# Performance work log

Measured on AMD Instinct MI355X. Metric: run time of the kernel, lower is better.

## Reference

```python
import jax, jax.numpy as jnp
import numpy as np

K = 8                      # batch_k
NONZERO_CUTOFF = 1.4       # nonzero_loss_cutoff
MARGIN = 1.0               # F.triplet_margin_loss default (module's margin arg is unused)
PD_EPS = 1e-6              # torch pairwise_distance eps


def setup_inputs() -> dict:
    key = jax.random.key(0)
    x = jax.random.normal(key, (4096, 128), dtype=jnp.float32)
    return {"x": x}


def _sample_indices(x, key):
    """Distance-weighted negative sampling; returns (a_idx, p_idx, n_idx), each [n*(K-1)]."""
    n, d = x.shape
    # per-row L2 normalize (eps added to norm, as in original)
    xn = x / (jnp.sqrt(jnp.sum(x * x, axis=1, keepdims=True)) + 1e-5)
    # pairwise euclidean distance; identity added under sqrt exactly as original
    sq = jnp.sum(xn * xn, axis=1, keepdims=True)               # [n,1]
    dist2 = sq + sq.T - 2.0 * (xn @ xn.T)                       # [n,n]
    dist = jnp.sqrt(dist2 + jnp.eye(n, dtype=x.dtype))          # [n,n]
    # distance-weighted sampling log-weights (Wu et al.)
    log_w = (2.0 - d) * jnp.log(dist) - (d - 3) / 2.0 * jnp.log(1.0 - 0.25 * dist * dist)
    w = jnp.exp(log_w - jnp.max(log_w))
    # block mask: same-block pairs excluded
    block = jnp.arange(n) // K                                  # [n]
    mask = (block[:, None] != block[None, :]).astype(x.dtype)
    w = w * mask * (dist < NONZERO_CUTOFF).astype(x.dtype)
    row_sum = jnp.sum(w, axis=1, keepdims=True)
    # rows where weights are degenerate fall back to uniform (original's try/except)
    valid = jnp.isfinite(row_sum) & (row_sum > 0) & jnp.all(jnp.isfinite(w), axis=1, keepdims=True)
    logits = jnp.where(valid, jnp.where(w > 0, jnp.log(w), -jnp.inf), 0.0)   # [n,n]
    # batched categorical sampling via Gumbel-max: K-1 negatives per anchor
    g = jax.random.gumbel(key, (n, K - 1, n), dtype=jnp.float32)
    n_idx = jnp.argmax(logits[:, None, :] + g, axis=-1).reshape(-1)          # [n*(K-1)]
    # anchor/positive pairs: for each i, all other members of its block
    r = jnp.arange(n) % K                                       # position in block
    off = jnp.arange(K - 1)
    p_off = jnp.where(off[None, :] < r[:, None], off[None, :], off[None, :] + 1)
    p_idx = (block[:, None] * K + p_off).reshape(-1)            # [n*(K-1)]
    a_idx = jnp.repeat(jnp.arange(n), K - 1)                    # [n*(K-1)]
    return a_idx, p_idx, n_idx


def reference(x) -> jnp.ndarray:
    key = jax.random.key(42)
    a_idx, p_idx, n_idx = _sample_indices(x, key)
    a, p, ng = x[a_idx], x[p_idx], x[n_idx]
    d_ap = jnp.sqrt(jnp.sum((a - p + PD_EPS) ** 2, axis=1))
    d_an = jnp.sqrt(jnp.sum((a - ng + PD_EPS) ** 2, axis=1))
    return jnp.mean(jnp.maximum(d_ap - d_an + MARGIN, 0.0))
```

## Files before the change

kernel.cpp:

```cpp
#include <hip/hip_runtime.h>
#include <stdint.h>

#define NROWS 4096
#define DIM   128
#define KB    8
#define NS    7
#define TCH   16
#define NPAIR 2048
#define HALF_CNT 58720256u

typedef __bf16 v8bf __attribute__((ext_vector_type(8)));
typedef float  v4f  __attribute__((ext_vector_type(4)));

__device__ __forceinline__ uint32_t rotl32(uint32_t x, int r) {
    return __builtin_amdgcn_alignbit(x, x, 32 - r);
}

__device__ __forceinline__ void threefry2x32(uint32_t c0, uint32_t c1,
                                             uint32_t& o0, uint32_t& o1) {
    const uint32_t ks0 = 0u;
    const uint32_t ks1 = 42u;
    const uint32_t ks2 = 0x1BD11BDAu ^ ks0 ^ ks1;
    uint32_t x0 = c0 + ks0;
    uint32_t x1 = c1 + ks1;
#define TF_R(r) { x0 += x1; x1 = rotl32(x1, r); x1 ^= x0; }
    TF_R(13) TF_R(15) TF_R(26) TF_R(6)
    x0 += ks1; x1 += ks2 + 1u;
    TF_R(17) TF_R(29) TF_R(16) TF_R(24)
    x0 += ks2; x1 += ks0 + 2u;
    TF_R(13) TF_R(15) TF_R(26) TF_R(6)
    x0 += ks0; x1 += ks1 + 3u;
    TF_R(17) TF_R(29) TF_R(16) TF_R(24)
    x0 += ks1; x1 += ks2 + 4u;
    TF_R(13) TF_R(15) TF_R(26) TF_R(6)
    x0 += ks2; x1 += ks0 + 5u;
#undef TF_R
    o0 = x0; o1 = x1;
}

__device__ __forceinline__ float gumbel_of(uint32_t b) {
    float f = __uint_as_float((b >> 9) | 0x3f800000u) - 1.0f;
    float u = f + 1.17549435e-38f;
    float l1 = __log2f(u);
    float inner = -0.69314718055994531f * l1;
    float l2 = __log2f(inner);
    return -0.69314718055994531f * l2;
}

__global__ void knorm(const float* __restrict__ x, __bf16* __restrict__ xb,
                      float* __restrict__ sqv) {
    const int i = blockIdx.x;
    const int t = threadIdx.x;
    float2 v = ((const float2*)(x + (size_t)i * DIM))[t];
    float s = v.x * v.x + v.y * v.y;
#pragma unroll
    for (int m = 32; m > 0; m >>= 1) s += __shfl_xor(s, m, 64);
    float norm = sqrtf(s) + 1e-5f;
    float ox = v.x / norm, oy = v.y / norm;
    union { __bf16 b[2]; uint32_t u; } ph;
    ph.b[0] = (__bf16)ox; ph.b[1] = (__bf16)oy;
    ((uint32_t*)xb)[i * 64 + t] = ph.u;
    float s2 = ox * ox + oy * oy;
#pragma unroll
    for (int m = 32; m > 0; m >>= 1) s2 += __shfl_xor(s2, m, 64);
    if (t == 0) sqv[i] = s2;
}

__global__ __launch_bounds__(256, 4) void kdist(
        const __bf16* __restrict__ xb, const float* __restrict__ sqv,
        int* __restrict__ cnt, unsigned short* __restrict__ t16,
        float2* __restrict__ nwp) {
    const int lane  = threadIdx.x & 63;
    const int chunk = (blockIdx.x << 2) + (threadIdx.x >> 6);
    const int grp   = blockIdx.y;
    const int rlo = lane & 15;
    const int khi = lane >> 4;
    const unsigned int below = (1u << rlo) - 1u;

    const int afr = grp * 8 + (rlo >> 1) + ((rlo & 1) << 11);
    v8bf ah[4];
#pragma unroll
    for (int ks = 0; ks < 4; ++ks)
        ah[ks] = *(const v8bf*)(xb + (size_t)afr * DIM + ks * 32 + khi * 8);

    const int base = grp * 8 + khi * 2;
    float sqA[4];
    sqA[0] = sqv[base];
    sqA[1] = sqv[base + 2048];
    sqA[2] = sqv[base + 1];
    sqA[3] = sqv[base + 2049];

    const int rbA = ((base)     * 16 + chunk) << 8;
    const int rbB = ((base + 1) * 16 + chunk) << 8;
    unsigned int cA = 0, cB = 0;

    const int tcol0 = chunk * 256 + rlo;

    v8bf bhn[4];
    float sqn;
    {
        const size_t boff = (size_t)tcol0 * DIM + khi * 8;
#pragma unroll
        for (int ks = 0; ks < 4; ++ks) bhn[ks] = *(const v8bf*)(xb + boff + ks * 32);
        sqn = sqv[tcol0];
    }

#pragma unroll 1
    for (int cg = 0; cg < 16; ++cg) {
        v8bf bhc[4];
#pragma unroll
        for (int ks = 0; ks < 4; ++ks) bhc[ks] = bhn[ks];
        const float sqB = sqn;
        const int tcol = tcol0 + cg * 16;

        if (cg < 15) {
            const size_t boff = (size_t)(tcol + 16) * DIM + khi * 8;
#pragma unroll
            for (int ks = 0; ks < 4; ++ks) bhn[ks] = *(const v8bf*)(xb + boff + ks * 32);
            sqn = sqv[tcol + 16];
        }

        v4f acc = {0.f, 0.f, 0.f, 0.f};
#pragma unroll
        for (int ks = 0; ks < 4; ++ks)
            acc = __builtin_amdgcn_mfma_f32_16x16x32_bf16(ah[ks], bhc[ks], acc, 0, 0, 0);

        const int tBlk = tcol >> 3;
        const bool bd0 = (tBlk != grp);
        const bool bd1 = (tBlk != grp + 256);

        float nw[4];
        bool  ic[4];
#pragma unroll
        for (int q = 0; q < 4; ++q) {
            float d2  = fmaf(-2.0f, acc[q], sqA[q] + sqB);
            float l1  = __log2f(d2);
            float t2  = fmaf(-0.25f, d2, 1.0f);
            float l2  = __log2f(t2);
            float wiv = exp2f(fmaf(63.0f, l1, 62.5f * l2));
            bool incl = (d2 < 1.96f) && ((q & 1) ? bd1 : bd0);
            ic[q] = incl;
            nw[q] = incl ? -wiv : -INFINITY;
        }

        const bool uA = ic[0] | ic[1];
        const bool uB = ic[2] | ic[3];
        unsigned long long ballA = __ballot(uA);
        unsigned long long ballB = __ballot(uB);
        unsigned int subA = (unsigned int)((ballA >> (khi * 16)) & 0xFFFFull);
        unsigned int subB = (unsigned int)((ballB >> (khi * 16)) & 0xFFFFull);
        if (uA) {
            int slot = rbA + (int)cA + __popc(subA & below);
            t16[slot] = (unsigned short)tcol;
            nwp[slot] = make_float2(nw[0], nw[1]);
        }
        if (uB) {
            int slot = rbB + (int)cB + __popc(subB & below);
            t16[slot] = (unsigned short)tcol;
            nwp[slot] = make_float2(nw[2], nw[3]);
        }
        cA += (unsigned int)__popc(subA);
        cB += (unsigned int)__popc(subB);
    }

    if (rlo == 0) {
        cnt[base * 16 + chunk]       = (int)cA;
        cnt[(base + 1) * 16 + chunk] = (int)cB;
    }
}

__global__ __launch_bounds__(256, 8) void kgum(
        const int* __restrict__ cnt, const unsigned short* __restrict__ t16,
        const float2* __restrict__ nwp,
        unsigned long long* __restrict__ pk) {
    const int wid  = threadIdx.x >> 6;
    const int rid  = (blockIdx.x << 2) + wid;
    const int p    = rid >> 4;
    const int lane = threadIdx.x & 63;
    const int j    = lane & 7;
    const int eo   = lane >> 3;
    const bool jv  = (j < 7);
    const uint32_t pb = ((uint32_t)p * 7u + (uint32_t)j) << 12;

    __shared__ unsigned short st[4][256];
    __shared__ float2         snw[4][256];

    const int n  = cnt[rid];
    const int rb = rid << 8;

    for (int s = lane; s < n; s += 64) {
        st[wid][s]  = t16[rb + s];
        snw[wid][s] = nwp[rb + s];
    }
    __syncthreads();

    unsigned long long bA = ~0ull, bB = ~0ull;

#pragma unroll 1
    for (int e = eo; e < n; e += 8) {
        const uint32_t t = st[wid][e];
        const float2 nw  = snw[wid][e];
        const uint32_t L = pb + t;
        uint32_t o0, o1;
        threefry2x32(L, L + HALF_CNT, o0, o1);
        float fA = __uint_as_float((o0 >> 9) | 0x3f800000u) - 1.0f;
        float fB = __uint_as_float((o1 >> 9) | 0x3f800000u) - 1.0f;
        float l1A = __log2f(fA + 1.17549435e-38f);
        float l1B = __log2f(fB + 1.17549435e-38f);
        float kA = jv ? l1A * nw.x : INFINITY;
        float kB = jv ? l1B * nw.y : INFINITY;
        unsigned long long pA = ((unsigned long long)__float_as_uint(kA) << 32) | t;
        unsigned long long pB = ((unsigned long long)__float_as_uint(kB) << 32) | t;
        bA = pA < bA ? pA : bA;
        bB = pB < bB ? pB : bB;
    }

#pragma unroll
    for (int m = 8; m < 64; m <<= 1) {
        unsigned long long vA = __shfl_xor(bA, m, 64);
        unsigned long long vB = __shfl_xor(bB, m, 64);
        bA = vA < bA ? vA : bA;
        bB = vB < bB ? vB : bB;
    }

    if (eo == 0 && jv) {
        atomicMin(&pk[(size_t)p * NS + j], bA);
        atomicMin(&pk[(size_t)(p + 2048) * NS + j], bB);
    }
}

__global__ void kextract(const unsigned long long* __restrict__ pk,
                         int* __restrict__ nidx) {
    int s = blockIdx.x * 256 + threadIdx.x;
    if (s >= NROWS * NS) return;
    unsigned long long v = pk[s];
    uint32_t kb = (uint32_t)(v >> 32);
    nidx[s] = (kb >= 0x7F800000u) ? -1 : (int)(v & 0xFFFFu);
}

__global__ __launch_bounds__(256, 2) void ksample(
        const __bf16* __restrict__ xb, const float* __restrict__ sqv,
        float* __restrict__ pV, int* __restrict__ pI) {
    const int lane  = threadIdx.x & 63;
    const int chunk = (blockIdx.x << 2) + (threadIdx.x >> 6);
    const int grp   = blockIdx.y;
    const int rlo = lane & 15;
    const int khi = lane >> 4;

    const int afr = grp * 8 + (rlo >> 1) + ((rlo & 1) << 11);
    v8bf ah[4];
#pragma unroll
    for (int ks = 0; ks < 4; ++ks)
        ah[ks] = *(const v8bf*)(xb + (size_t)afr * DIM + ks * 32 + khi * 8);
    const int base = grp * 8 + khi * 2;
    float sqA[4];
    sqA[0] = sqv[base];
    sqA[1] = sqv[base + 2048];
    sqA[2] = sqv[base + 1];
    sqA[3] = sqv[base + 2049];
    const uint32_t P0 = (uint32_t)base;
    const uint32_t P1 = (uint32_t)(base + 1);

    float    bestV[4][NS];
    uint32_t bestP[4];
#pragma unroll
    for (int q = 0; q < 4; ++q) {
        bestP[q] = 0u;
#pragma unroll
        for (int j = 0; j < NS; ++j) bestV[q][j] = INFINITY;
    }
    const int tcol0 = chunk * 256 + rlo;

    v8bf bhn[4];
    float sqn;
    {
        const size_t boff = (size_t)tcol0 * DIM + khi * 8;
#pragma unroll
        for (int ks = 0; ks < 4; ++ks) bhn[ks] = *(const v8bf*)(xb + boff + ks * 32);
        sqn = sqv[tcol0];
    }

#pragma unroll 1
    for (int cg = 0; cg < 16; ++cg) {
        v8bf bhc[4];
#pragma unroll
        for (int ks = 0; ks < 4; ++ks) bhc[ks] = bhn[ks];
        const float sqB = sqn;
        const int tcol = tcol0 + cg * 16;
        if (cg < 15) {
            const size_t boff = (size_t)(tcol + 16) * DIM + khi * 8;
#pragma unroll
            for (int ks = 0; ks < 4; ++ks) bhn[ks] = *(const v8bf*)(xb + boff + ks * 32);
            sqn = sqv[tcol + 16];
        }
        v4f acc = {0.f, 0.f, 0.f, 0.f};
#pragma unroll
        for (int ks = 0; ks < 4; ++ks)
            acc = __builtin_amdgcn_mfma_f32_16x16x32_bf16(ah[ks], bhc[ks], acc, 0, 0, 0);
        const int tBlk = tcol >> 3;
        const bool bd0 = (tBlk != grp);
        const bool bd1 = (tBlk != grp + 256);
        float nw[4];
#pragma unroll
        for (int q = 0; q < 4; ++q) {
            float d2  = fmaf(-2.0f, acc[q], sqA[q] + sqB);
            float l1  = __log2f(d2);
            float t2  = fmaf(-0.25f, d2, 1.0f);
            float l2  = __log2f(t2);
            float wiv = exp2f(fmaf(63.0f, l1, 62.5f * l2));
            bool incl = (d2 < 1.96f) && ((q & 1) ? bd1 : bd0);
            nw[q] = incl ? -wiv : -INFINITY;
        }
        const uint32_t tB = (uint32_t)tcol;
#pragma unroll
        for (int j = 0; j < NS; ++j) {
            uint32_t L0 = ((P0 * 7u + (uint32_t)j) << 12) + tB;
            uint32_t L1 = ((P1 * 7u + (uint32_t)j) << 12) + tB;
            uint32_t o0, o1, o2, o3;
            threefry2x32(L0, L0 + HALF_CNT, o0, o1);
            threefry2x32(L1, L1 + HALF_CNT, o2, o3);
            float vv[4];
            vv[0] = __log2f(__uint_as_float((o0 >> 9) | 0x3f800000u) - 1.0f + 1.17549435e-38f) * nw[0];
            vv[1] = __log2f(__uint_as_float((o1 >> 9) | 0x3f800000u) - 1.0f + 1.17549435e-38f) * nw[1];
            vv[2] = __log2f(__uint_as_float((o2 >> 9) | 0x3f800000u) - 1.0f + 1.17549435e-38f) * nw[2];
            vv[3] = __log2f(__uint_as_float((o3 >> 9) | 0x3f800000u) - 1.0f + 1.17549435e-38f) * nw[3];
            const uint32_t keep = ~(0xFu << (4 * j));
            const uint32_t put  = ((uint32_t)cg) << (4 * j);
#pragma unroll
            for (int q = 0; q < 4; ++q) {
                bool lt = vv[q] < bestV[q][j];
                uint32_t np = (bestP[q] & keep) | put;
                bestV[q][j] = lt ? vv[q] : bestV[q][j];
                bestP[q]    = lt ? np : bestP[q];
            }
        }
    }
#pragma unroll
    for (int q = 0; q < 4; ++q) {
        const int a = base + (q >> 1) + ((q & 1) << 11);
#pragma unroll
        for (int j = 0; j < NS; ++j) {
            float v = bestV[q][j];
            int idx = tcol0 + (int)((bestP[q] >> (4 * j)) & 0xFu) * 16;
#pragma unroll
            for (int m = 1; m < 16; m <<= 1) {
                float v2 = __shfl_xor(v, m, 16);
                int   i2 = __shfl_xor(idx, m, 16);
                if (v2 < v || (v2 == v && i2 < idx)) { v = v2; idx = i2; }
            }
            if (rlo == 0) {
                size_t s = ((size_t)a * NS + j) * TCH + chunk;
                pV[s] = v;
                pI[s] = idx;
            }
        }
    }
}

__global__ void kcombine(const float* __restrict__ pV, const int* __restrict__ pI,
                         int* __restrict__ nidx, int nc) {
    int s = blockIdx.x * 256 + threadIdx.x;
    if (s >= NROWS * NS) return;
    float bv = INFINITY;
    int bi = 0x7FFFFFFF;
    for (int c = 0; c < nc; ++c) {
        float v = pV[(size_t)s * nc + c];
        int idx = pI[(size_t)s * nc + c];
        if (v < bv || (v == bv && idx < bi)) { bv = v; bi = idx; }
    }
    nidx[s] = (bv == INFINITY) ? -1 : bi;
}

__global__ void kfixup(int* __restrict__ nidx) {
    const int i = blockIdx.x;
    if (nidx[(size_t)i * NS] >= 0) return;
    const int lane = threadIdx.x;
    for (int j = 0; j < NS; ++j) {
        float bv = -INFINITY;
        int bi = 0x7FFFFFFF;
        for (int t = lane; t < NROWS; t += 64) {
            uint32_t o0, o1;
            float g;
            if (i < 2048) {
                uint32_t L = (((uint32_t)(i * NS + j)) << 12) + (uint32_t)t;
                threefry2x32(L, L + HALF_CNT, o0, o1);
                g = gumbel_of(o0);
            } else {
                uint32_t L = (((uint32_t)((i - 2048) * NS + j)) << 12) + (uint32_t)t;
                threefry2x32(L, L + HALF_CNT, o0, o1);
                g = gumbel_of(o1);
            }
            if (g > bv) { bv = g; bi = t; }
        }
#pragma unroll
        for (int m = 1; m < 64; m <<= 1) {
            float v2 = __shfl_xor(bv, m, 64);
            int   i2 = __shfl_xor(bi, m, 64);
            if (v2 > bv || (v2 == bv && i2 < bi)) { bv = v2; bi = i2; }
        }
        if (lane == 0) nidx[i * NS + j] = bi;
    }
}

__global__ void kloss(const float* __restrict__ x, const int* __restrict__ nidx,
                      float* __restrict__ loss) {
    int s = blockIdx.x * 256 + threadIdx.x;
    if (s >= NROWS * NS) return;
    int i = s / NS, j = s - i * NS;
    int r = i & (KB - 1), blk = i >> 3;
    int po = (j < r) ? j : j + 1;
    int p = blk * KB + po;
    int n = nidx[s] & (NROWS - 1);
    const float4* A  = (const float4*)(x + (size_t)i * DIM);
    const float4* P  = (const float4*)(x + (size_t)p * DIM);
    const float4* Ng = (const float4*)(x + (size_t)n * DIM);
    float sap = 0.0f, san = 0.0f;
#pragma unroll 8
    for (int k = 0; k < DIM / 4; ++k) {
        float4 a = A[k], pv = P[k], nv = Ng[k];
        float d;
        d = a.x - pv.x + 1e-6f; sap += d * d;
        d = a.y - pv.y + 1e-6f; sap += d * d;
        d = a.z - pv.z + 1e-6f; sap += d * d;
        d = a.w - pv.w + 1e-6f; sap += d * d;
        d = a.x - nv.x + 1e-6f; san += d * d;
        d = a.y - nv.y + 1e-6f; san += d * d;
        d = a.z - nv.z + 1e-6f; san += d * d;
        d = a.w - nv.w + 1e-6f; san += d * d;
    }
    loss[s] = fmaxf(sqrtf(sap) - sqrtf(san) + 1.0f, 0.0f);
}

__global__ void kreduce(const float* __restrict__ loss, float* __restrict__ out) {
    __shared__ float part[4];
    const int tid = threadIdx.x;
    float sum = 0.0f;
    for (int s = tid; s < NROWS * NS; s += 256) sum += loss[s];
#pragma unroll
    for (int m = 32; m > 0; m >>= 1) sum += __shfl_xor(sum, m, 64);
    if ((tid & 63) == 0) part[tid >> 6] = sum;
    __syncthreads();
    if (tid == 0) out[0] = (part[0] + part[1] + part[2] + part[3]) / 28672.0f;
}

extern "C" void kernel_launch(void* const* d_in, const int* in_sizes, int n_in,
                              void* d_out, int out_size, void* d_ws, size_t ws_size,
                              hipStream_t stream) {
    const float* x = (const float*)d_in[0];
    float* out = (float*)d_out;

    uint8_t* w = (uint8_t*)d_ws;
    size_t off = 0;
    auto take = [&](size_t bytes) {
        void* p = w + off;
        off = (off + bytes + 255) & ~(size_t)255;
        return p;
    };
    __bf16* xb   = (__bf16*)take((size_t)NROWS * DIM * 2);
    float*  sqv  = (float*)take((size_t)NROWS * 4);
    int*    nidx = (int*)take((size_t)NROWS * NS * 4);
    float*  loss = (float*)take((size_t)NROWS * NS * 4);
    int*    cnt  = (int*)take((size_t)NPAIR * 16 * 4);
    unsigned long long* pk = (unsigned long long*)take((size_t)NROWS * NS * 8);
    const size_t prefix = off;
    const size_t t16_b = (size_t)NPAIR * 16 * 256 * 2;
    const size_t nwp_b = (size_t)NPAIR * 16 * 256 * 8;
    const size_t NEED_BIG = prefix + ((t16_b + 255) & ~(size_t)255)
                          + ((nwp_b + 255) & ~(size_t)255);

    knorm<<<NROWS, 64, 0, stream>>>(x, xb, sqv);

    if (ws_size >= NEED_BIG) {
        unsigned short* t16 = (unsigned short*)take(t16_b);
        float2*         nwp = (float2*)take(nwp_b);
        hipMemsetAsync(pk, 0xFF, (size_t)NROWS * NS * 8, stream);
        kdist<<<dim3(TCH / 4, 256), 256, 0, stream>>>(xb, sqv, cnt, t16, nwp);
        kgum<<<NPAIR * 16 / 4, 256, 0, stream>>>(cnt, t16, nwp, pk);
        kextract<<<(NROWS * NS + 255) / 256, 256, 0, stream>>>(pk, nidx);
    } else {
        float* pV = (float*)take((size_t)NROWS * NS * TCH * 4);
        int*   pI = (int*)take((size_t)NROWS * NS * TCH * 4);
        ksample<<<dim3(TCH / 4, 256), 256, 0, stream>>>(xb, sqv, pV, pI);
        kcombine<<<(NROWS * NS + 255) / 256, 256, 0, stream>>>(pV, pI, nidx, TCH);
    }

    kfixup<<<NROWS, 64, 0, stream>>>(nidx);
    kloss<<<(NROWS * NS + 255) / 256, 256, 0, stream>>>(x, nidx, loss);
    kreduce<<<1, 256, 0, stream>>>(loss, out);
}
```

Baseline: 198.8 us.

## Restructure Gumbel kernel to one block per pair, drop atomics and extract pass

The Gumbel-max kernel now assigns one block per anchor pair. Each thread loops over all 7 samples for each candidate, so every candidate is loaded once instead of through a lane-per-sample split that left one of eight lanes idle. Per-sample minima are reduced with wave shuffles and then across waves in shared memory, and the block writes nidx directly. This removes the memset, the 64-bit global atomicMin and the separate extract kernel. In exchange each thread needs more registers for 14 running minima, the launch bound drops to 4 blocks, and there are fewer blocks overall.

```diff
diff --git a/kernel.cpp b/kernel.cpp
--- a/kernel.cpp
+++ b/kernel.cpp
@@ -169,73 +169,75 @@
     }
 }
 
-__global__ __launch_bounds__(256, 8) void kgum(
+__global__ __launch_bounds__(256, 4) void kgum(
         const int* __restrict__ cnt, const unsigned short* __restrict__ t16,
-        const float2* __restrict__ nwp,
-        unsigned long long* __restrict__ pk) {
+        const float2* __restrict__ nwp, int* __restrict__ nidx) {
+    const int p    = blockIdx.x;
     const int wid  = threadIdx.x >> 6;
-    const int rid  = (blockIdx.x << 2) + wid;
-    const int p    = rid >> 4;
     const int lane = threadIdx.x & 63;
-    const int j    = lane & 7;
-    const int eo   = lane >> 3;
-    const bool jv  = (j < 7);
-    const uint32_t pb = ((uint32_t)p * 7u + (uint32_t)j) << 12;
-
-    __shared__ unsigned short st[4][256];
-    __shared__ float2         snw[4][256];
-
-    const int n  = cnt[rid];
-    const int rb = rid << 8;
-
-    for (int s = lane; s < n; s += 64) {
-        st[wid][s]  = t16[rb + s];
-        snw[wid][s] = nwp[rb + s];
+    const uint32_t pb0 = ((uint32_t)p * 7u) << 12;
+
+    unsigned long long bA[NS], bB[NS];
+#pragma unroll
+    for (int j = 0; j < NS; ++j) { bA[j] = ~0ull; bB[j] = ~0ull; }
+
+#pragma unroll 1
+    for (int c = wid * 4; c < wid * 4 + 4; ++c) {
+        const int rid = p * 16 + c;
+        const int n  = cnt[rid];
+        const int rb = rid << 8;
+#pragma unroll 1
+        for (int e = lane; e < n; e += 64) {
+            const uint32_t t = t16[rb + e];
+            const float2 nw  = nwp[rb + e];
+#pragma unroll
+            for (int j = 0; j < NS; ++j) {
+                const uint32_t L = pb0 + ((uint32_t)j << 12) + t;
+                uint32_t o0, o1;
+                threefry2x32(L, L + HALF_CNT, o0, o1);
+                float fA = __uint_as_float((o0 >> 9) | 0x3f800000u) - 1.0f;
+                float fB = __uint_as_float((o1 >> 9) | 0x3f800000u) - 1.0f;
+                float kA = __log2f(fA + 1.17549435e-38f) * nw.x;
+                float kB = __log2f(fB + 1.17549435e-38f) * nw.y;
+                unsigned long long pA =
+                    ((unsigned long long)__float_as_uint(kA) << 32) | t;
+                unsigned long long pB =
+                    ((unsigned long long)__float_as_uint(kB) << 32) | t;
+                bA[j] = pA < bA[j] ? pA : bA[j];
+                bB[j] = pB < bB[j] ? pB : bB[j];
+            }
+        }
+    }
+
+#pragma unroll
+    for (int j = 0; j < NS; ++j) {
+#pragma unroll
+        for (int m = 1; m < 64; m <<= 1) {
+            unsigned long long vA = __shfl_xor(bA[j], m, 64);
+            unsigned long long vB = __shfl_xor(bB[j], m, 64);
+            bA[j] = vA < bA[j] ? vA : bA[j];
+            bB[j] = vB < bB[j] ? vB : bB[j];
+        }
+    }
+
+    __shared__ unsigned long long sA[4][NS], sB[4][NS];
+    if (lane == 0) {
+#pragma unroll
+        for (int j = 0; j < NS; ++j) { sA[wid][j] = bA[j]; sB[wid][j] = bB[j]; }
     }
     __syncthreads();
-
-    unsigned long long bA = ~0ull, bB = ~0ull;
-
-#pragma unroll 1
-    for (int e = eo; e < n; e += 8) {
-        const uint32_t t = st[wid][e];
-        const float2 nw  = snw[wid][e];
-        const uint32_t L = pb + t;
-        uint32_t o0, o1;
-        threefry2x32(L, L + HALF_CNT, o0, o1);
-        float fA = __uint_as_float((o0 >> 9) | 0x3f800000u) - 1.0f;
-        float fB = __uint_as_float((o1 >> 9) | 0x3f800000u) - 1.0f;
-        float l1A = __log2f(fA + 1.17549435e-38f);
-        float l1B = __log2f(fB + 1.17549435e-38f);
-        float kA = jv ? l1A * nw.x : INFINITY;
-        float kB = jv ? l1B * nw.y : INFINITY;
-        unsigned long long pA = ((unsigned long long)__float_as_uint(kA) << 32) | t;
-        unsigned long long pB = ((unsigned long long)__float_as_uint(kB) << 32) | t;
-        bA = pA < bA ? pA : bA;
-        bB = pB < bB ? pB : bB;
-    }
-
-#pragma unroll
-    for (int m = 8; m < 64; m <<= 1) {
-        unsigned long long vA = __shfl_xor(bA, m, 64);
-        unsigned long long vB = __shfl_xor(bB, m, 64);
-        bA = vA < bA ? vA : bA;
-        bB = vB < bB ? vB : bB;
-    }
-
-    if (eo == 0 && jv) {
-        atomicMin(&pk[(size_t)p * NS + j], bA);
-        atomicMin(&pk[(size_t)(p + 2048) * NS + j], bB);
-    }
-}
-
-__global__ void kextract(const unsigned long long* __restrict__ pk,
-                         int* __restrict__ nidx) {
-    int s = blockIdx.x * 256 + threadIdx.x;
-    if (s >= NROWS * NS) return;
-    unsigned long long v = pk[s];
-    uint32_t kb = (uint32_t)(v >> 32);
-    nidx[s] = (kb >= 0x7F800000u) ? -1 : (int)(v & 0xFFFFu);
+    if (threadIdx.x < 2 * NS) {
+        const int r = threadIdx.x / NS, j = threadIdx.x - r * NS;
+        unsigned long long v = r ? sB[0][j] : sA[0][j];
+#pragma unroll
+        for (int w = 1; w < 4; ++w) {
+            unsigned long long v2 = r ? sB[w][j] : sA[w][j];
+            v = v2 < v ? v2 : v;
+        }
+        uint32_t kb = (uint32_t)(v >> 32);
+        nidx[(p + r * 2048) * NS + j] = (kb >= 0x7F800000u) ? -1
+                                                            : (int)(v & 0xFFFFu);
+    }
 }
 
 __global__ __launch_bounds__(256, 2) void ksample(
@@ -461,7 +463,6 @@
     int*    nidx = (int*)take((size_t)NROWS * NS * 4);
     float*  loss = (float*)take((size_t)NROWS * NS * 4);
     int*    cnt  = (int*)take((size_t)NPAIR * 16 * 4);
-    unsigned long long* pk = (unsigned long long*)take((size_t)NROWS * NS * 8);
     const size_t prefix = off;
     const size_t t16_b = (size_t)NPAIR * 16 * 256 * 2;
     const size_t nwp_b = (size_t)NPAIR * 16 * 256 * 8;
@@ -473,10 +474,8 @@
     if (ws_size >= NEED_BIG) {
         unsigned short* t16 = (unsigned short*)take(t16_b);
         float2*         nwp = (float2*)take(nwp_b);
-        hipMemsetAsync(pk, 0xFF, (size_t)NROWS * NS * 8, stream);
         kdist<<<dim3(TCH / 4, 256), 256, 0, stream>>>(xb, sqv, cnt, t16, nwp);
-        kgum<<<NPAIR * 16 / 4, 256, 0, stream>>>(cnt, t16, nwp, pk);
-        kextract<<<(NROWS * NS + 255) / 256, 256, 0, stream>>>(pk, nidx);
+        kgum<<<NPAIR, 256, 0, stream>>>(cnt, t16, nwp, nidx);
     } else {
         float* pV = (float*)take((size_t)NROWS * NS * TCH * 4);
         int*   pI = (int*)take((size_t)NROWS * NS * TCH * 4);
```

New measurement: 189.3 us. -4.8%, faster.
